# Kernel optimization log

Hardware: AMD Instinct MI355X
Metric: run time of the kernel (lower is better)

## Reference

```python
import jax, jax.numpy as jnp
import numpy as np

NA = 50000   # nodes of type 'a'
NB = 50000   # nodes of type 'b'
E = 800000   # edges per cross relation
D = 256      # input feature dim == hidden_dim (SAGEConv lazy in-dim)
H = 256      # hidden_dim
EMB = 128    # embedding_dim
L = 2        # num_layer
# relation order in stacked weights: 0=(a,to,b), 1=(b,to,a), 2=(a,self_loop,a), 3=(b,self_loop,b)


def setup_inputs() -> dict:
    key = jax.random.key(0)
    ks = jax.random.split(key, 8)
    x_a = jax.random.normal(ks[0], (NA, D), jnp.float32)
    x_b = jax.random.normal(ks[1], (NB, D), jnp.float32)
    edge_ab = jax.random.randint(ks[2], (2, E), 0, NA, dtype=jnp.int32)  # row0: src in a, row1: dst in b
    edge_ba = jax.random.randint(ks[3], (2, E), 0, NB, dtype=jnp.int32)  # row0: src in b, row1: dst in a
    s = 1.0 / np.sqrt(H)
    Wl = jax.random.normal(ks[4], (L, 4, H, H), jnp.float32) * s  # lin_l weight (on aggregated neighbors)
    bl = jnp.zeros((L, 4, H), jnp.float32)                         # lin_l bias
    Wr = jax.random.normal(ks[5], (L, 4, H, H), jnp.float32) * s  # lin_r weight (root/self), no bias
    lin_W = jax.random.normal(ks[6], (H, EMB), jnp.float32) * s
    lin_b = jnp.zeros((EMB,), jnp.float32)
    return dict(x_a=x_a, x_b=x_b, edge_ab=edge_ab, edge_ba=edge_ba,
                Wl=Wl, bl=bl, Wr=Wr, lin_W=lin_W, lin_b=lin_b)


def _sage(x_src, x_dst, src, dst, n_dst, Wl, bl, Wr):
    # SAGEConv: mean-aggregate neighbor features, then lin_l(agg) + lin_r(x_dst)
    agg = jax.ops.segment_sum(x_src[src], dst, num_segments=n_dst)           # [n_dst, H]
    cnt = jax.ops.segment_sum(jnp.ones(src.shape, x_src.dtype), dst, num_segments=n_dst)
    mean = agg / jnp.maximum(cnt, 1.0)[:, None]                               # isolated dst -> 0
    return mean @ Wl + bl + x_dst @ Wr


def _sage_self(x, Wl, bl, Wr):
    # self-loop relation: each node has exactly one neighbor (itself), mean == x
    return x @ Wl + bl + x @ Wr


def reference(x_a, x_b, edge_ab, edge_ba, Wl, bl, Wr, lin_W, lin_b):
    xa, xb = x_a, x_b
    for l in range(L):
        new_a = (_sage(xb, xa, edge_ba[0], edge_ba[1], xa.shape[0], Wl[l, 1], bl[l, 1], Wr[l, 1])
                 + _sage_self(xa, Wl[l, 2], bl[l, 2], Wr[l, 2]))
        new_b = (_sage(xa, xb, edge_ab[0], edge_ab[1], xb.shape[0], Wl[l, 0], bl[l, 0], Wr[l, 0])
                 + _sage_self(xb, Wl[l, 3], bl[l, 3], Wr[l, 3]))
        xa, xb = jax.nn.relu(new_a), jax.nn.relu(new_b)
    return xa @ lin_W + lin_b, xb @ lin_W + lin_b
```

## Files before the change

kernel.cpp:

```cpp
#include <hip/hip_runtime.h>
#include <hip/hip_bf16.h>

#define NNA 50000
#define NNB 50000
#define NE  800000
#define HD  256
#define EMBD 128

typedef __attribute__((ext_vector_type(4))) int            i32x4;
typedef __attribute__((ext_vector_type(4))) float          f32x4;
typedef __attribute__((ext_vector_type(8))) short          bf16x8;
typedef __attribute__((ext_vector_type(4))) unsigned short u16x4;
typedef __attribute__((ext_vector_type(8))) unsigned short u16x8;

static __device__ __forceinline__ float bf2f(unsigned short u) {
  union { unsigned int i; float f; } v; v.i = ((unsigned int)u) << 16; return v.f;
}
static __device__ __forceinline__ unsigned short f2bf(float f) {
  __hip_bfloat16 h = __float2bfloat16(f);
  return *reinterpret_cast<unsigned short*>(&h);
}

static __device__ __forceinline__ void gload_lds16(const void* g, void* l) {
  __builtin_amdgcn_global_load_lds((const __attribute__((address_space(1))) void*)g,
                                   (__attribute__((address_space(3))) void*)l, 16, 0, 0);
}

__global__ void k_prep(const float* __restrict__ Wl, const float* __restrict__ Wr,
                       const float* __restrict__ bl, const float* __restrict__ linW,
                       unsigned short* __restrict__ WcatT, float* __restrict__ bias,
                       unsigned short* __restrict__ linWT) {
  int id = blockIdx.x * 256 + threadIdx.x;
  if (id < 2 * 2 * 512 * 256) {
    int n = id & 255;
    int k = (id >> 8) & 511;
    int t = (id >> 17) & 1;
    int l = id >> 18;
    int rn = (t == 0) ? 1 : 0;
    int rs = (t == 0) ? 2 : 3;
    float v;
    if (k < HD) {
      v = Wl[((l * 4 + rn) * HD + k) * HD + n];
    } else {
      int kk = k - HD;
      v = Wr[((l * 4 + rn) * HD + kk) * HD + n]
        + Wl[((l * 4 + rs) * HD + kk) * HD + n]
        + Wr[((l * 4 + rs) * HD + kk) * HD + n];
    }
    WcatT[((l * 2 + t) * HD + n) * 512 + k] = f2bf(v);
    return;
  }
  int id1 = id - 2 * 2 * 512 * 256;
  if (id1 < 2 * 2 * 256) {
    int n = id1 & 255; int t = (id1 >> 8) & 1; int l = id1 >> 9;
    int rn = (t == 0) ? 1 : 0;
    int rs = (t == 0) ? 2 : 3;
    bias[id1] = bl[(l * 4 + rn) * HD + n] + bl[(l * 4 + rs) * HD + n];
    return;
  }
  int id2 = id1 - 2 * 2 * 256;
  if (id2 < EMBD * HD) {
    int k = id2 & 255; int n = id2 >> 8;
    linWT[n * HD + k] = f2bf(linW[k * EMBD + n]);
  }
}

__global__ void k_convert(const float* __restrict__ xa, const float* __restrict__ xb,
                          unsigned short* __restrict__ out) {
  const int n4a = NNA * HD / 4;
  const int n4  = (NNA + NNB) * HD / 4;
  int i = blockIdx.x * blockDim.x + threadIdx.x;
  int stride = gridDim.x * blockDim.x;
  for (; i < n4; i += stride) {
    const float* src = (i < n4a) ? (xa + (size_t)i * 4) : (xb + (size_t)(i - n4a) * 4);
    f32x4 v = *reinterpret_cast<const f32x4*>(src);
    u16x4 o;
    o[0] = f2bf(v[0]); o[1] = f2bf(v[1]); o[2] = f2bf(v[2]); o[3] = f2bf(v[3]);
    reinterpret_cast<u16x4*>(out)[i] = o;
  }
}

__global__ void k_fill(const int* __restrict__ e_ba, const int* __restrict__ e_ab,
                       int* __restrict__ cnt_a, int* __restrict__ slots_a,
                       int* __restrict__ cnt_b, int* __restrict__ slots_b) {
  int e = blockIdx.x * 256 + threadIdx.x;
  if (e < NE) {
    int src = e_ba[e];
    int dst = e_ba[NE + e];
    int pos = atomicAdd(&cnt_a[dst], 1);
    if (pos < 64) slots_a[dst * 64 + pos] = src;
  } else if (e < 2 * NE) {
    int f = e - NE;
    int src = e_ab[f];
    int dst = e_ab[NE + f];
    int pos = atomicAdd(&cnt_b[dst], 1);
    if (pos < 64) slots_b[dst * 64 + pos] = src;
  }
}

__global__ __launch_bounds__(256)
void k_aggregate(const unsigned short* __restrict__ xa,
                 const unsigned short* __restrict__ xb,
                 const int* __restrict__ slots_a, const int* __restrict__ cnt_a,
                 const int* __restrict__ slots_b, const int* __restrict__ cnt_b,
                 unsigned short* __restrict__ mean_a, unsigned short* __restrict__ mean_b) {
  int w = blockIdx.x * 4 + (threadIdx.x >> 6);
  int lane = threadIdx.x & 63;
  const unsigned short* xsrc;
  const int* sl;
  int deg;
  unsigned short* outp;
  if (w < NNA) {
    xsrc = xb; sl = slots_a + (size_t)w * 64; deg = cnt_a[w];
    outp = mean_a + (size_t)w * HD;
  } else {
    int v = w - NNA;
    xsrc = xa; sl = slots_b + (size_t)v * 64; deg = cnt_b[v];
    outp = mean_b + (size_t)v * HD;
  }
  int m = deg < 64 ? deg : 64;
  int s_all = sl[lane];
  const int half = lane >> 5;
  const int l31 = lane & 31;

  float acc[8];
#pragma unroll
  for (int k = 0; k < 8; ++k) acc[k] = 0.f;

  int j = 0;
  for (; j + 8 <= m; j += 8) {
    int sj[4];
#pragma unroll
    for (int i = 0; i < 4; ++i) sj[i] = __shfl(s_all, j + 2 * i + half);
    u16x8 v[4];
#pragma unroll
    for (int i = 0; i < 4; ++i)
      v[i] = *reinterpret_cast<const u16x8*>(xsrc + (size_t)sj[i] * HD + l31 * 8);
#pragma unroll
    for (int i = 0; i < 4; ++i)
#pragma unroll
      for (int k = 0; k < 8; ++k) acc[k] += bf2f(v[i][k]);
  }
  for (; j + 2 <= m; j += 2) {
    int sj = __shfl(s_all, j + half);
    u16x8 v = *reinterpret_cast<const u16x8*>(xsrc + (size_t)sj * HD + l31 * 8);
#pragma unroll
    for (int k = 0; k < 8; ++k) acc[k] += bf2f(v[k]);
  }
  if (j < m && half == 0) {
    int sj = __shfl(s_all, j);
    u16x8 v = *reinterpret_cast<const u16x8*>(xsrc + (size_t)sj * HD + l31 * 8);
#pragma unroll
    for (int k = 0; k < 8; ++k) acc[k] += bf2f(v[k]);
  }

#pragma unroll
  for (int k = 0; k < 8; ++k) acc[k] += __shfl_xor(acc[k], 32);

  float inv = deg > 0 ? 1.0f / (float)deg : 0.0f;
  if (half == 0) {
    u16x8 o;
#pragma unroll
    for (int k = 0; k < 8; ++k) o[k] = f2bf(acc[k] * inv);
    *reinterpret_cast<u16x8*>(outp + l31 * 8) = o;
  }
}

template <bool RELU, bool OUTF32>
__global__ __launch_bounds__(256)
void k_gemm(const unsigned short* __restrict__ Alo,
            const unsigned short* __restrict__ Ahi,
            const unsigned short* __restrict__ BT,
            const float* __restrict__ bias,
            void* __restrict__ Cout,
            int M, int N, int Ktot, int Klo,
            long long sA, long long sB, long long sBias, long long sCbytes) {
  const int z = blockIdx.z;
  Alo += (long long)z * sA;
  Ahi += (long long)z * sA;
  BT += (long long)z * sB;
  bias += (long long)z * sBias;
  Cout = (void*)((char*)Cout + (long long)z * sCbytes);

  __shared__ char smem[65536];
  const int t = threadIdx.x;
  const int bm = blockIdx.x, bn = blockIdx.y;
  const int lane = t & 63, wid = t >> 6;
  const int wm = wid >> 1, wn = wid & 1;
  const int l15 = lane & 15, l4 = lane >> 4;
  const int rgrp = lane >> 3;
  const int boff = (((lane & 7) ^ rgrp) << 4);

  f32x4 acc[4][4];
#pragma unroll
  for (int i = 0; i < 4; ++i)
#pragma unroll
    for (int j = 0; j < 4; ++j) acc[i][j] = (f32x4){0.f, 0.f, 0.f, 0.f};

  const int nks = Ktot >> 6;

  auto stage = [&](int ks, int buf) {
    const int kglob = ks << 6;
    const unsigned short* Asrc = (kglob < Klo) ? Alo : Ahi;
    const int kbase = (kglob < Klo) ? kglob : (kglob - Klo);
    char* sA_ = smem + buf * 16384;
    char* sB_ = smem + 32768 + buf * 16384;
#pragma unroll
    for (int i = 0; i < 4; ++i) {
      int rloc = wid * 32 + i * 8;
      int rA = bm * 128 + rloc + rgrp;
      if (rA >= M) rA = M - 1;
      const char* ga = (const char*)(Asrc + (size_t)rA * HD + kbase) + boff;
      gload_lds16(ga, sA_ + rloc * 128);
      int rB = bn * 128 + rloc + rgrp;
      const char* gb = (const char*)(BT + (size_t)rB * Ktot + kglob) + boff;
      gload_lds16(gb, sB_ + rloc * 128);
    }
  };

  stage(0, 0);
  __syncthreads();

  for (int ks = 0; ks < nks; ++ks) {
    if (ks + 1 < nks) stage(ks + 1, (ks + 1) & 1);
    const char* sA_ = smem + (ks & 1) * 16384;
    const char* sB_ = smem + 32768 + (ks & 1) * 16384;
#pragma unroll
    for (int kk = 0; kk < 2; ++kk) {
      bf16x8 af[4], bfr[4];
#pragma unroll
      for (int f = 0; f < 4; ++f) {
        int r = wm * 64 + f * 16 + l15;
        af[f] = *reinterpret_cast<const bf16x8*>(
            sA_ + r * 128 + ((kk * 64 + l4 * 16) ^ ((r & 7) << 4)));
        int n = wn * 64 + f * 16 + l15;
        bfr[f] = *reinterpret_cast<const bf16x8*>(
            sB_ + n * 128 + ((kk * 64 + l4 * 16) ^ ((n & 7) << 4)));
      }
#pragma unroll
      for (int fm = 0; fm < 4; ++fm)
#pragma unroll
        for (int fn = 0; fn < 4; ++fn)
          acc[fm][fn] = __builtin_amdgcn_mfma_f32_16x16x32_bf16(af[fm], bfr[fn], acc[fm][fn], 0, 0, 0);
    }
    __syncthreads();
  }

#pragma unroll
  for (int fm = 0; fm < 4; ++fm) {
    int row0 = bm * 128 + wm * 64 + fm * 16 + l4 * 4;
#pragma unroll
    for (int fn = 0; fn < 4; ++fn) {
      int col = bn * 128 + wn * 64 + fn * 16 + l15;
      float bv = bias[col];
      f32x4 d = acc[fm][fn];
#pragma unroll
      for (int r = 0; r < 4; ++r) {
        int rg = row0 + r;
        if (rg < M) {
          float v = d[r] + bv;
          if (RELU) v = v > 0.f ? v : 0.f;
          if (OUTF32)
            reinterpret_cast<float*>(Cout)[(size_t)rg * N + col] = v;
          else
            reinterpret_cast<unsigned short*>(Cout)[(size_t)rg * N + col] = f2bf(v);
        }
      }
    }
  }
}


extern "C" void kernel_launch(void* const* d_in, const int* in_sizes, int n_in,
                              void* d_out, int out_size, void* d_ws, size_t ws_size,
                              hipStream_t stream) {
  const float* x_a  = (const float*)d_in[0];
  const float* x_b  = (const float*)d_in[1];
  const int*   e_ab = (const int*)d_in[2];
  const int*   e_ba = (const int*)d_in[3];
  const float* Wl   = (const float*)d_in[4];
  const float* bl   = (const float*)d_in[5];
  const float* Wr   = (const float*)d_in[6];
  const float* linW = (const float*)d_in[7];
  const float* linb = (const float*)d_in[8];
  float* out = (float*)d_out;

  char* ws = (char*)d_ws;
  size_t off = 0;
  auto alloc = [&](size_t bytes) {
    char* p = ws + off;
    off += (bytes + 255) & ~(size_t)255;
    return p;
  };
  unsigned short* x0   = (unsigned short*)alloc((size_t)2 * NNA * HD * 2);
  unsigned short* x1   = (unsigned short*)alloc((size_t)2 * NNA * HD * 2);
  unsigned short* mean = (unsigned short*)alloc((size_t)2 * NNA * HD * 2);
  int* slots_a = (int*)alloc((size_t)NNA * 64 * 4);
  int* slots_b = (int*)alloc((size_t)NNB * 64 * 4);
  int* cnt_a   = (int*)alloc((size_t)NNA * 4);
  int* cnt_b   = (int*)alloc((size_t)NNB * 4);
  unsigned short* wcatT  = (unsigned short*)alloc((size_t)2 * 2 * 256 * 512 * 2);
  float*          biasv  = (float*)alloc((size_t)2 * 2 * 256 * 4);
  unsigned short* linWT  = (unsigned short*)alloc((size_t)EMBD * HD * 2);
  (void)ws_size; (void)in_sizes; (void)n_in; (void)out_size;

  hipMemsetAsync(cnt_a, 0, (size_t)NNA * 4, stream);
  hipMemsetAsync(cnt_b, 0, (size_t)NNB * 4, stream);

  k_prep<<<(2 * 2 * 512 * 256 + 1024 + 32768 + 255) / 256, 256, 0, stream>>>(
      Wl, Wr, bl, linW, wcatT, biasv, linWT);
  k_convert<<<2048, 256, 0, stream>>>(x_a, x_b, x0);
  k_fill<<<(2 * NE + 255) / 256, 256, 0, stream>>>(e_ba, e_ab, cnt_a, slots_a, cnt_b, slots_b);

  unsigned short* xcur = x0;
  unsigned short* xnxt = x1;

  for (int l = 0; l < 2; ++l) {
    k_aggregate<<<(NNA + NNB) / 4, 256, 0, stream>>>(
        xcur, xcur + (size_t)NNA * HD, slots_a, cnt_a, slots_b, cnt_b,
        mean, mean + (size_t)NNA * HD);
    dim3 g((NNA + 127) / 128, 2, 2);
    k_gemm<true, false><<<g, 256, 0, stream>>>(
        mean, xcur, wcatT + (size_t)l * 2 * 256 * 512, biasv + l * 2 * 256, xnxt,
        NNA, 256, 512, 256,
        (long long)NNA * HD, 256 * 512, 256, (long long)NNA * HD * 2);
    unsigned short* tmp = xcur; xcur = xnxt; xnxt = tmp;
  }

  dim3 gf((NNA + 127) / 128, 1, 2);
  k_gemm<false, true><<<gf, 256, 0, stream>>>(
      xcur, xcur, linWT, linb, out,
      NNA, EMBD, 256, 256,
      (long long)NNA * HD, 0, 0, (long long)NNA * EMBD * 4);
}
```

Before: 527.5 us.

## Fuse front-end kernels, switch to fp16, shrink slot indices to 16-bit

Merges the convert, CSR-fill and weight-prep kernels into one launch and unifies the a/b count and slot arrays so a single memset clears them. Slot indices are stored as 16-bit values, halving slot traffic; this only holds because node counts fit in 16 bits. Feature storage and MFMA switch from bf16 to fp16, trading dynamic range for mantissa precision, so large values could overflow. Cost is a heterogeneous front-end kernel with branchy block roles.

```diff
diff --git a/kernel.cpp b/kernel.cpp
--- a/kernel.cpp
+++ b/kernel.cpp
@@ -6,19 +6,26 @@
 #define NE  800000
 #define HD  256
 #define EMBD 128
+#define NDST (NNA + NNB)
+
+#define CONV_BLOCKS 2048
+#define FILL_BLOCKS ((2 * NE) / 256)
+#define PREP_IDS (2 * 2 * 512 * 256 + 1024 + 32768)
+#define PREP_BLOCKS ((PREP_IDS + 255) / 256)
 
 typedef __attribute__((ext_vector_type(4))) int            i32x4;
 typedef __attribute__((ext_vector_type(4))) float          f32x4;
-typedef __attribute__((ext_vector_type(8))) short          bf16x8;
+typedef __attribute__((ext_vector_type(8))) _Float16       f16x8;
 typedef __attribute__((ext_vector_type(4))) unsigned short u16x4;
 typedef __attribute__((ext_vector_type(8))) unsigned short u16x8;
 
-static __device__ __forceinline__ float bf2f(unsigned short u) {
-  union { unsigned int i; float f; } v; v.i = ((unsigned int)u) << 16; return v.f;
-}
-static __device__ __forceinline__ unsigned short f2bf(float f) {
-  __hip_bfloat16 h = __float2bfloat16(f);
-  return *reinterpret_cast<unsigned short*>(&h);
+static __device__ __forceinline__ float h2f(unsigned short u) {
+  _Float16 h = __builtin_bit_cast(_Float16, u);
+  return (float)h;
+}
+static __device__ __forceinline__ unsigned short f2h(float f) {
+  _Float16 h = (_Float16)f;
+  return __builtin_bit_cast(unsigned short, h);
 }
 
 static __device__ __forceinline__ void gload_lds16(const void* g, void* l) {
@@ -26,100 +33,104 @@
                                    (__attribute__((address_space(3))) void*)l, 16, 0, 0);
 }
 
-__global__ void k_prep(const float* __restrict__ Wl, const float* __restrict__ Wr,
-                       const float* __restrict__ bl, const float* __restrict__ linW,
-                       unsigned short* __restrict__ WcatT, float* __restrict__ bias,
-                       unsigned short* __restrict__ linWT) {
-  int id = blockIdx.x * 256 + threadIdx.x;
-  if (id < 2 * 2 * 512 * 256) {
-    int n = id & 255;
-    int k = (id >> 8) & 511;
-    int t = (id >> 17) & 1;
-    int l = id >> 18;
-    int rn = (t == 0) ? 1 : 0;
-    int rs = (t == 0) ? 2 : 3;
-    float v;
-    if (k < HD) {
-      v = Wl[((l * 4 + rn) * HD + k) * HD + n];
+__global__ __launch_bounds__(256)
+void k_front(const float* __restrict__ xa, const float* __restrict__ xb,
+             unsigned short* __restrict__ xout,
+             const int* __restrict__ e_ba, const int* __restrict__ e_ab,
+             int* __restrict__ cnt, unsigned short* __restrict__ slots,
+             const float* __restrict__ Wl, const float* __restrict__ Wr,
+             const float* __restrict__ bl, const float* __restrict__ linW,
+             unsigned short* __restrict__ WcatT, float* __restrict__ bias,
+             unsigned short* __restrict__ linWT) {
+  int b = blockIdx.x;
+  if (b < CONV_BLOCKS) {
+    const int n4a = NNA * HD / 4;
+    const int n4  = (NNA + NNB) * HD / 4;
+    int i = b * 256 + threadIdx.x;
+    const int stride = CONV_BLOCKS * 256;
+    for (; i < n4; i += stride) {
+      const float* src = (i < n4a) ? (xa + (size_t)i * 4) : (xb + (size_t)(i - n4a) * 4);
+      f32x4 v = *reinterpret_cast<const f32x4*>(src);
+      u16x4 o;
+      o[0] = f2h(v[0]); o[1] = f2h(v[1]); o[2] = f2h(v[2]); o[3] = f2h(v[3]);
+      reinterpret_cast<u16x4*>(xout)[i] = o;
+    }
+    return;
+  }
+  b -= CONV_BLOCKS;
+  if (b < FILL_BLOCKS) {
+    int e = b * 256 + threadIdx.x;
+    int src, gdst;
+    if (e < NE) {
+      src = e_ba[e];
+      gdst = e_ba[NE + e];
     } else {
-      int kk = k - HD;
-      v = Wr[((l * 4 + rn) * HD + kk) * HD + n]
-        + Wl[((l * 4 + rs) * HD + kk) * HD + n]
-        + Wr[((l * 4 + rs) * HD + kk) * HD + n];
-    }
-    WcatT[((l * 2 + t) * HD + n) * 512 + k] = f2bf(v);
+      int f = e - NE;
+      src = e_ab[f];
+      gdst = NNA + e_ab[NE + f];
+    }
+    int pos = atomicAdd(&cnt[gdst], 1);
+    if (pos < 64) slots[(size_t)gdst * 64 + pos] = (unsigned short)src;
     return;
   }
-  int id1 = id - 2 * 2 * 512 * 256;
-  if (id1 < 2 * 2 * 256) {
-    int n = id1 & 255; int t = (id1 >> 8) & 1; int l = id1 >> 9;
-    int rn = (t == 0) ? 1 : 0;
-    int rs = (t == 0) ? 2 : 3;
-    bias[id1] = bl[(l * 4 + rn) * HD + n] + bl[(l * 4 + rs) * HD + n];
-    return;
-  }
-  int id2 = id1 - 2 * 2 * 256;
-  if (id2 < EMBD * HD) {
-    int k = id2 & 255; int n = id2 >> 8;
-    linWT[n * HD + k] = f2bf(linW[k * EMBD + n]);
-  }
-}
-
-__global__ void k_convert(const float* __restrict__ xa, const float* __restrict__ xb,
-                          unsigned short* __restrict__ out) {
-  const int n4a = NNA * HD / 4;
-  const int n4  = (NNA + NNB) * HD / 4;
-  int i = blockIdx.x * blockDim.x + threadIdx.x;
-  int stride = gridDim.x * blockDim.x;
-  for (; i < n4; i += stride) {
-    const float* src = (i < n4a) ? (xa + (size_t)i * 4) : (xb + (size_t)(i - n4a) * 4);
-    f32x4 v = *reinterpret_cast<const f32x4*>(src);
-    u16x4 o;
-    o[0] = f2bf(v[0]); o[1] = f2bf(v[1]); o[2] = f2bf(v[2]); o[3] = f2bf(v[3]);
-    reinterpret_cast<u16x4*>(out)[i] = o;
-  }
-}
-
-__global__ void k_fill(const int* __restrict__ e_ba, const int* __restrict__ e_ab,
-                       int* __restrict__ cnt_a, int* __restrict__ slots_a,
-                       int* __restrict__ cnt_b, int* __restrict__ slots_b) {
-  int e = blockIdx.x * 256 + threadIdx.x;
-  if (e < NE) {
-    int src = e_ba[e];
-    int dst = e_ba[NE + e];
-    int pos = atomicAdd(&cnt_a[dst], 1);
-    if (pos < 64) slots_a[dst * 64 + pos] = src;
-  } else if (e < 2 * NE) {
-    int f = e - NE;
-    int src = e_ab[f];
-    int dst = e_ab[NE + f];
-    int pos = atomicAdd(&cnt_b[dst], 1);
-    if (pos < 64) slots_b[dst * 64 + pos] = src;
+  b -= FILL_BLOCKS;
+  {
+    int id = b * 256 + threadIdx.x;
+    if (id < 2 * 2 * 512 * 256) {
+      int n = id & 255;
+      int k = (id >> 8) & 511;
+      int t = (id >> 17) & 1;
+      int l = id >> 18;
+      int rn = (t == 0) ? 1 : 0;
+      int rs = (t == 0) ? 2 : 3;
+      float v;
+      if (k < HD) {
+        v = Wl[((l * 4 + rn) * HD + k) * HD + n];
+      } else {
+        int kk = k - HD;
+        v = Wr[((l * 4 + rn) * HD + kk) * HD + n]
+          + Wl[((l * 4 + rs) * HD + kk) * HD + n]
+          + Wr[((l * 4 + rs) * HD + kk) * HD + n];
+      }
+      WcatT[((l * 2 + t) * HD + n) * 512 + k] = f2h(v);
+      return;
+    }
+    int id1 = id - 2 * 2 * 512 * 256;
+    if (id1 < 2 * 2 * 256) {
+      int n = id1 & 255; int t = (id1 >> 8) & 1; int l = id1 >> 9;
+      int rn = (t == 0) ? 1 : 0;
+      int rs = (t == 0) ? 2 : 3;
+      bias[id1] = bl[(l * 4 + rn) * HD + n] + bl[(l * 4 + rs) * HD + n];
+      return;
+    }
+    int id2 = id1 - 2 * 2 * 256;
+    if (id2 < EMBD * HD) {
+      int k = id2 & 255; int n = id2 >> 8;
+      linWT[n * HD + k] = f2h(linW[k * EMBD + n]);
+    }
   }
 }
 
 __global__ __launch_bounds__(256)
 void k_aggregate(const unsigned short* __restrict__ xa,
                  const unsigned short* __restrict__ xb,
-                 const int* __restrict__ slots_a, const int* __restrict__ cnt_a,
-                 const int* __restrict__ slots_b, const int* __restrict__ cnt_b,
+                 const unsigned short* __restrict__ slots,
+                 const int* __restrict__ cnt,
                  unsigned short* __restrict__ mean_a, unsigned short* __restrict__ mean_b) {
   int w = blockIdx.x * 4 + (threadIdx.x >> 6);
   int lane = threadIdx.x & 63;
   const unsigned short* xsrc;
-  const int* sl;
-  int deg;
   unsigned short* outp;
+  int deg = cnt[w];
   if (w < NNA) {
-    xsrc = xb; sl = slots_a + (size_t)w * 64; deg = cnt_a[w];
+    xsrc = xb;
     outp = mean_a + (size_t)w * HD;
   } else {
-    int v = w - NNA;
-    xsrc = xa; sl = slots_b + (size_t)v * 64; deg = cnt_b[v];
-    outp = mean_b + (size_t)v * HD;
+    xsrc = xa;
+    outp = mean_b + (size_t)(w - NNA) * HD;
   }
   int m = deg < 64 ? deg : 64;
-  int s_all = sl[lane];
+  int s_all = (int)slots[(size_t)w * 64 + lane];
   const int half = lane >> 5;
   const int l31 = lane & 31;
 
@@ -139,19 +150,19 @@
 #pragma unroll
     for (int i = 0; i < 4; ++i)
 #pragma unroll
-      for (int k = 0; k < 8; ++k) acc[k] += bf2f(v[i][k]);
+      for (int k = 0; k < 8; ++k) acc[k] += h2f(v[i][k]);
   }
   for (; j + 2 <= m; j += 2) {
     int sj = __shfl(s_all, j + half);
     u16x8 v = *reinterpret_cast<const u16x8*>(xsrc + (size_t)sj * HD + l31 * 8);
 #pragma unroll
-    for (int k = 0; k < 8; ++k) acc[k] += bf2f(v[k]);
+    for (int k = 0; k < 8; ++k) acc[k] += h2f(v[k]);
   }
   if (j < m && half == 0) {
     int sj = __shfl(s_all, j);
     u16x8 v = *reinterpret_cast<const u16x8*>(xsrc + (size_t)sj * HD + l31 * 8);
 #pragma unroll
-    for (int k = 0; k < 8; ++k) acc[k] += bf2f(v[k]);
+    for (int k = 0; k < 8; ++k) acc[k] += h2f(v[k]);
   }
 
 #pragma unroll
@@ -161,7 +172,7 @@
   if (half == 0) {
     u16x8 o;
 #pragma unroll
-    for (int k = 0; k < 8; ++k) o[k] = f2bf(acc[k] * inv);
+    for (int k = 0; k < 8; ++k) o[k] = f2h(acc[k] * inv);
     *reinterpret_cast<u16x8*>(outp + l31 * 8) = o;
   }
 }
@@ -227,21 +238,21 @@
     const char* sB_ = smem + 32768 + (ks & 1) * 16384;
 #pragma unroll
     for (int kk = 0; kk < 2; ++kk) {
-      bf16x8 af[4], bfr[4];
+      f16x8 af[4], bfr[4];
 #pragma unroll
       for (int f = 0; f < 4; ++f) {
         int r = wm * 64 + f * 16 + l15;
-        af[f] = *reinterpret_cast<const bf16x8*>(
+        af[f] = *reinterpret_cast<const f16x8*>(
             sA_ + r * 128 + ((kk * 64 + l4 * 16) ^ ((r & 7) << 4)));
         int n = wn * 64 + f * 16 + l15;
-        bfr[f] = *reinterpret_cast<const bf16x8*>(
+        bfr[f] = *reinterpret_cast<const f16x8*>(
             sB_ + n * 128 + ((kk * 64 + l4 * 16) ^ ((n & 7) << 4)));
       }
 #pragma unroll
       for (int fm = 0; fm < 4; ++fm)
 #pragma unroll
         for (int fn = 0; fn < 4; ++fn)
-          acc[fm][fn] = __builtin_amdgcn_mfma_f32_16x16x32_bf16(af[fm], bfr[fn], acc[fm][fn], 0, 0, 0);
+          acc[fm][fn] = __builtin_amdgcn_mfma_f32_16x16x32_f16(af[fm], bfr[fn], acc[fm][fn], 0, 0, 0);
     }
     __syncthreads();
   }
@@ -263,7 +274,7 @@
           if (OUTF32)
             reinterpret_cast<float*>(Cout)[(size_t)rg * N + col] = v;
           else
-            reinterpret_cast<unsigned short*>(Cout)[(size_t)rg * N + col] = f2bf(v);
+            reinterpret_cast<unsigned short*>(Cout)[(size_t)rg * N + col] = f2h(v);
         }
       }
     }
@@ -295,29 +306,24 @@
   unsigned short* x0   = (unsigned short*)alloc((size_t)2 * NNA * HD * 2);
   unsigned short* x1   = (unsigned short*)alloc((size_t)2 * NNA * HD * 2);
   unsigned short* mean = (unsigned short*)alloc((size_t)2 * NNA * HD * 2);
-  int* slots_a = (int*)alloc((size_t)NNA * 64 * 4);
-  int* slots_b = (int*)alloc((size_t)NNB * 64 * 4);
-  int* cnt_a   = (int*)alloc((size_t)NNA * 4);
-  int* cnt_b   = (int*)alloc((size_t)NNB * 4);
+  int*            cnt  = (int*)alloc((size_t)NDST * 4);
+  unsigned short* slots = (unsigned short*)alloc((size_t)NDST * 64 * 2);
   unsigned short* wcatT  = (unsigned short*)alloc((size_t)2 * 2 * 256 * 512 * 2);
   float*          biasv  = (float*)alloc((size_t)2 * 2 * 256 * 4);
   unsigned short* linWT  = (unsigned short*)alloc((size_t)EMBD * HD * 2);
   (void)ws_size; (void)in_sizes; (void)n_in; (void)out_size;
 
-  hipMemsetAsync(cnt_a, 0, (size_t)NNA * 4, stream);
-  hipMemsetAsync(cnt_b, 0, (size_t)NNB * 4, stream);
-
-  k_prep<<<(2 * 2 * 512 * 256 + 1024 + 32768 + 255) / 256, 256, 0, stream>>>(
-      Wl, Wr, bl, linW, wcatT, biasv, linWT);
-  k_convert<<<2048, 256, 0, stream>>>(x_a, x_b, x0);
-  k_fill<<<(2 * NE + 255) / 256, 256, 0, stream>>>(e_ba, e_ab, cnt_a, slots_a, cnt_b, slots_b);
+  hipMemsetAsync(cnt, 0, (size_t)NDST * 4, stream);
+
+  k_front<<<CONV_BLOCKS + FILL_BLOCKS + PREP_BLOCKS, 256, 0, stream>>>(
+      x_a, x_b, x0, e_ba, e_ab, cnt, slots, Wl, Wr, bl, linW, wcatT, biasv, linWT);
 
   unsigned short* xcur = x0;
   unsigned short* xnxt = x1;
 
   for (int l = 0; l < 2; ++l) {
     k_aggregate<<<(NNA + NNB) / 4, 256, 0, stream>>>(
-        xcur, xcur + (size_t)NNA * HD, slots_a, cnt_a, slots_b, cnt_b,
+        xcur, xcur + (size_t)NNA * HD, slots, cnt,
         mean, mean + (size_t)NNA * HD);
     dim3 g((NNA + 127) / 128, 2, 2);
     k_gemm<true, false><<<g, 256, 0, stream>>>(
```

New measurement: 527.9 us. About the same (+0.1%).
